# Kernel optimization log

Measured on AMD Instinct MI355X. Metric: run time of the kernel, lower is better.

## Reference

```python
import jax, jax.numpy as jnp
import numpy as np

DIM_V = 512
NUM_HEADS = 8
LN_EPS = 1e-5


def _layernorm(x):
    # LayerNorm over last dim, no affine (simplified_layer_norm=True)
    mu = jnp.mean(x, axis=-1, keepdims=True)
    var = jnp.mean(jnp.square(x - mu), axis=-1, keepdims=True)
    return (x - mu) * jax.lax.rsqrt(var + LN_EPS)


def setup_inputs() -> dict:
    key = jax.random.key(0)
    ks = jax.random.split(key, 12)
    B, Nq, Nk, dQ, dK, dV = 16, 1024, 1024, 512, 512, DIM_V
    s = 0.02
    return {
        "Q": jax.random.normal(ks[0], (B, Nq, dQ), jnp.float32),
        "K": jax.random.normal(ks[1], (B, Nk, dK), jnp.float32),
        "Wq": jax.random.normal(ks[2], (dQ, dV), jnp.float32) * s,
        "bq": jnp.zeros((dV,), jnp.float32),
        "Wk": jax.random.normal(ks[3], (dK, dV), jnp.float32) * s,
        "bk": jnp.zeros((dV,), jnp.float32),
        "Wv": jax.random.normal(ks[4], (dK, dV), jnp.float32) * s,
        "bv": jnp.zeros((dV,), jnp.float32),
        "Wo": jax.random.normal(ks[5], (dV, dV), jnp.float32) * s,
        "bo": jnp.zeros((dV,), jnp.float32),
    }


def reference(Q, K, Wq, bq, Wk, bk, Wv, bv, Wo, bo):
    H = NUM_HEADS
    dh = DIM_V // H
    q = Q @ Wq + bq            # [B, Nq, dV]
    k = K @ Wk + bk            # [B, Nk, dV]
    v = K @ Wv + bv            # [B, Nk, dV]
    B, Nq, _ = q.shape
    Nk = k.shape[1]
    qh = q.reshape(B, Nq, H, dh)
    kh = k.reshape(B, Nk, H, dh)
    vh = v.reshape(B, Nk, H, dh)
    # NOTE: faithful to source — scale by sqrt(dim_V), not sqrt(head_dim)
    scores = jnp.einsum('bqhd,bkhd->bhqk', qh, kh) / jnp.sqrt(jnp.asarray(DIM_V, q.dtype))
    A = jax.nn.softmax(scores, axis=-1)                    # [B, H, Nq, Nk]
    attn = jnp.einsum('bhqk,bkhd->bqhd', A, vh).reshape(B, Nq, DIM_V)
    O = q + attn               # residual with projected Q
    O = _layernorm(O)          # ln0 (no affine)
    O = O + jax.nn.gelu(O @ Wo + bo, approximate=False)
    O = _layernorm(O)          # ln1 (no affine)
    return O
```

## Files before the change

### kernel.cpp

```cpp
#include <hip/hip_runtime.h>
#include <hip/hip_bf16.h>
#include <math.h>

typedef __bf16 bf16;
typedef __bf16 bf16x8 __attribute__((ext_vector_type(8)));
typedef __bf16 bf16x4 __attribute__((ext_vector_type(4)));
typedef float  f32x4  __attribute__((ext_vector_type(4)));

#define MFMA16(a,b,c) __builtin_amdgcn_mfma_f32_16x16x32_bf16((a),(b),(c),0,0,0)
#define ATT_SCALE 0.0441941738241592f

__device__ __forceinline__ void async16(const bf16* g, bf16* l) {
    __builtin_amdgcn_global_load_lds((const __attribute__((address_space(1))) void*)g,
                                     (__attribute__((address_space(3))) void*)l,
                                     16, 0, 0);
}

__global__ __launch_bounds__(256) void prep_kernel(
    const float* __restrict__ Q, const float* __restrict__ K,
    const float* __restrict__ Wq, const float* __restrict__ Wk,
    const float* __restrict__ Wv, const float* __restrict__ Wo,
    bf16* __restrict__ Qb, bf16* __restrict__ Kb,
    bf16* __restrict__ WqT, bf16* __restrict__ WkT,
    bf16* __restrict__ WvT, bf16* __restrict__ WoT)
{
    __shared__ float tile[32][33];
    const int bx = blockIdx.x;
    if (bx < 8192) {
        const float* src = (bx < 4096) ? Q : K;
        bf16* dst        = (bx < 4096) ? Qb : Kb;
        int i = ((bx & 4095) * 256 + threadIdx.x) * 8;
        float4 a = *(const float4*)(src + i);
        float4 b = *(const float4*)(src + i + 4);
        bf16x8 o;
        o[0]=(bf16)a.x; o[1]=(bf16)a.y; o[2]=(bf16)a.z; o[3]=(bf16)a.w;
        o[4]=(bf16)b.x; o[5]=(bf16)b.y; o[6]=(bf16)b.z; o[7]=(bf16)b.w;
        *(bf16x8*)(dst + i) = o;
    } else {
        const int wid = bx - 8192;
        const float* W; bf16* T;
        switch (wid >> 8) {
          case 0: W=Wq; T=WqT; break;
          case 1: W=Wk; T=WkT; break;
          case 2: W=Wv; T=WvT; break;
          default: W=Wo; T=WoT; break;
        }
        const int rest = wid & 255;
        const int k0 = (rest & 15) * 32, n0 = (rest >> 4) * 32;
        const int tx = threadIdx.x & 31, ty = threadIdx.x >> 5;
        #pragma unroll
        for (int i=0;i<32;i+=8)
            tile[ty+i][tx] = W[(size_t)(k0+ty+i)*512 + n0+tx];
        __syncthreads();
        #pragma unroll
        for (int i=0;i<32;i+=8)
            T[(size_t)(n0+ty+i)*512 + k0+tx] = (bf16)tile[tx][ty+i];
    }
}

__device__ __forceinline__ void gemm_bt_body(
    const bf16* __restrict__ A, const bf16* __restrict__ BT,
    const float* __restrict__ bias,
    float* __restrict__ Cf, bf16* __restrict__ Cb, bf16* __restrict__ CvT)
{
    __shared__ bf16 As[128][32];
    __shared__ bf16 Bs[128][32];
    __shared__ bf16 Lt[64][136];
    const int m0 = blockIdx.x * 128, n0 = blockIdx.y * 128;
    const int tid = threadIdx.x;
    const int lane = tid & 63, wave = tid >> 6;
    const int qd = lane >> 4, lr = lane & 15;
    const int wm = (wave & 1) * 64, wn = (wave >> 1) * 64;

    const bf16* gA = A  + (size_t)(m0 + (tid>>2))*512 + (tid&3)*8;
    const bf16* gB = BT + (size_t)(n0 + (tid>>2))*512 + (tid&3)*8;
    bf16* lA = &As[0][0] + wave*512;
    bf16* lB = &Bs[0][0] + wave*512;

    f32x4 acc[4][4];
    #pragma unroll
    for (int i=0;i<4;i++)
      #pragma unroll
      for (int j=0;j<4;j++) acc[i][j] = (f32x4){0.f,0.f,0.f,0.f};

    for (int k0 = 0; k0 < 512; k0 += 32) {
        __syncthreads();
        async16(gA + k0,            lA);
        async16(gA + 64*512 + k0,   lA + 2048);
        async16(gB + k0,            lB);
        async16(gB + 64*512 + k0,   lB + 2048);
        __syncthreads();
        bf16x8 af[4], bfr[4];
        #pragma unroll
        for (int mi=0;mi<4;mi++) af[mi]  = *(bf16x8*)(&As[wm + mi*16 + lr][qd*8]);
        #pragma unroll
        for (int ni=0;ni<4;ni++) bfr[ni] = *(bf16x8*)(&Bs[wn + ni*16 + lr][qd*8]);
        #pragma unroll
        for (int mi=0;mi<4;mi++)
          #pragma unroll
          for (int ni=0;ni<4;ni++)
            acc[mi][ni] = MFMA16(af[mi], bfr[ni], acc[mi][ni]);
    }

    if (Cf || Cb) {
        #pragma unroll
        for (int ni=0;ni<4;ni++) {
            int n = n0 + wn + ni*16 + lr;
            float bv = bias[n];
            #pragma unroll
            for (int mi=0;mi<4;mi++) {
                int mb = m0 + wm + mi*16 + qd*4;
                #pragma unroll
                for (int r=0;r<4;r++) {
                    float v = acc[mi][ni][r] + bv;
                    if (Cf) Cf[(size_t)(mb+r)*512 + n] = v;
                    if (Cb) Cb[(size_t)(mb+r)*512 + n] = (bf16)v;
                }
            }
        }
    }
    if (CvT) {
        const int b = m0 >> 10, tok0 = m0 & 1023;
        const int row = tid >> 2, ch = tid & 3;
        #pragma unroll
        for (int half = 0; half < 2; ++half) {
            __syncthreads();
            if ((wn >> 6) == half) {
                #pragma unroll
                for (int ni=0;ni<4;ni++) {
                    int nl = ni*16 + lr;
                    float bv = bias[n0 + half*64 + nl];
                    #pragma unroll
                    for (int mi=0;mi<4;mi++)
                      #pragma unroll
                      for (int r=0;r<4;r++)
                        Lt[nl][wm + mi*16 + qd*4 + r] = (bf16)(acc[mi][ni][r] + bv);
                }
            }
            __syncthreads();
            const int h = (n0 >> 6) + half;
            uint4 x0 = *(uint4*)(&Lt[row][ch*32]);
            uint4 x1 = *(uint4*)(&Lt[row][ch*32 + 8]);
            bf16* dst = CvT + ((size_t)((b*8 + h)*64 + row))*1024 + tok0 + ch*32;
            *(uint4*)dst       = x0;
            *(uint4*)(dst + 8) = x1;
        }
    }
}

__global__ __launch_bounds__(256) void gemm_proj_kernel(
    const bf16* __restrict__ Qb, const bf16* __restrict__ Kb,
    const bf16* __restrict__ WqT, const bf16* __restrict__ WkT, const bf16* __restrict__ WvT,
    const float* __restrict__ bq, const float* __restrict__ bk, const float* __restrict__ bv,
    bf16* __restrict__ qbb, bf16* __restrict__ kbb, bf16* __restrict__ vT)
{
    switch (blockIdx.z) {
      case 0:  gemm_bt_body(Qb, WqT, bq, nullptr, qbb, nullptr); break;
      case 1:  gemm_bt_body(Kb, WkT, bk, nullptr, kbb, nullptr); break;
      default: gemm_bt_body(Kb, WvT, bv, nullptr, nullptr, vT); break;
    }
}

__global__ __launch_bounds__(256) void gemm_o_kernel(
    const bf16* __restrict__ Obf, const bf16* __restrict__ WoT,
    const float* __restrict__ bo, float* __restrict__ G32)
{
    gemm_bt_body(Obf, WoT, bo, G32, nullptr, nullptr);
}

__global__ __launch_bounds__(256, 4) void attn_kernel(
    const bf16* __restrict__ qb, const bf16* __restrict__ kb,
    const bf16* __restrict__ vT, bf16* __restrict__ attnb)
{
    const int qt = blockIdx.x, h = blockIdx.y, b = blockIdx.z;
    const int tid = threadIdx.x, lane = tid & 63, wave = tid >> 6;
    const int qd = lane >> 4, lr = lane & 15;
    const int q0 = qt*128 + wave*32;

    __shared__ bf16 Ks[64][72];
    __shared__ bf16 Vs[64][72];
    __shared__ bf16 Pl[4][32][72];

    bf16x8 aq[2][2];
    #pragma unroll
    for (int mi=0;mi<2;mi++) {
        const bf16* qrow = qb + ((size_t)(b*1024 + q0 + mi*16 + lr))*512 + h*64;
        aq[mi][0] = *(const bf16x8*)(qrow + qd*8);
        aq[mi][1] = *(const bf16x8*)(qrow + 32 + qd*8);
    }

    const int srow = tid >> 2;
    const int scol = (tid & 3) * 16;
    const bf16* kgp = kb + ((size_t)(b*1024 + srow))*512 + h*64 + scol;
    const bf16* vgp = vT + ((size_t)((b*8 + h)*64 + srow))*1024 + scol;

    uint4 k0r = *(const uint4*)(kgp);
    uint4 k1r = *(const uint4*)(kgp + 8);
    uint4 v0r = *(const uint4*)(vgp);
    uint4 v1r = *(const uint4*)(vgp + 8);

    f32x4 acc[2][4];
    #pragma unroll
    for (int mi=0;mi<2;mi++)
      #pragma unroll
      for (int ni=0;ni<4;ni++) acc[mi][ni] = (f32x4){0.f,0.f,0.f,0.f};
    float l[2][4] = {{0.f,0.f,0.f,0.f},{0.f,0.f,0.f,0.f}};

    for (int t=0; t<16; ++t) {
        __syncthreads();
        *(uint4*)(&Ks[srow][scol])   = k0r;
        *(uint4*)(&Ks[srow][scol+8]) = k1r;
        *(uint4*)(&Vs[srow][scol])   = v0r;
        *(uint4*)(&Vs[srow][scol+8]) = v1r;
        __syncthreads();
        if (t < 15) {
            const size_t ko = (size_t)(t+1)*64*512;
            const size_t vo = (size_t)(t+1)*64;
            k0r = *(const uint4*)(kgp + ko);
            k1r = *(const uint4*)(kgp + ko + 8);
            v0r = *(const uint4*)(vgp + vo);
            v1r = *(const uint4*)(vgp + vo + 8);
        }

        f32x4 s[2][4];
        #pragma unroll
        for (int mi=0;mi<2;mi++)
          #pragma unroll
          for (int ni=0;ni<4;ni++) s[mi][ni] = (f32x4){0.f,0.f,0.f,0.f};
        #pragma unroll
        for (int ni=0;ni<4;ni++) {
            bf16x8 b0 = *(bf16x8*)(&Ks[ni*16+lr][qd*8]);
            bf16x8 b1 = *(bf16x8*)(&Ks[ni*16+lr][32+qd*8]);
            #pragma unroll
            for (int mi=0;mi<2;mi++) {
                s[mi][ni] = MFMA16(aq[mi][0], b0, s[mi][ni]);
                s[mi][ni] = MFMA16(aq[mi][1], b1, s[mi][ni]);
            }
        }
        #pragma unroll
        for (int mi=0;mi<2;mi++)
          #pragma unroll
          for (int ni=0;ni<4;ni++)
            #pragma unroll
            for (int r=0;r<4;r++) {
                float pv = __expf(s[mi][ni][r] * ATT_SCALE);
                s[mi][ni][r] = pv;
                l[mi][r] += pv;
            }
        #pragma unroll
        for (int mi=0;mi<2;mi++)
          #pragma unroll
          for (int ni=0;ni<4;ni++)
            #pragma unroll
            for (int r=0;r<4;r++)
                Pl[wave][mi*16 + qd*4 + r][ni*16 + lr] = (bf16)s[mi][ni][r];
        bf16x8 ap[2][2];
        #pragma unroll
        for (int mi=0;mi<2;mi++) {
            ap[mi][0] = *(bf16x8*)(&Pl[wave][mi*16+lr][qd*8]);
            ap[mi][1] = *(bf16x8*)(&Pl[wave][mi*16+lr][32+qd*8]);
        }
        #pragma unroll
        for (int ni=0;ni<4;ni++) {
            bf16x8 v0 = *(bf16x8*)(&Vs[ni*16+lr][qd*8]);
            bf16x8 v1 = *(bf16x8*)(&Vs[ni*16+lr][32+qd*8]);
            #pragma unroll
            for (int mi=0;mi<2;mi++) {
                acc[mi][ni] = MFMA16(ap[mi][0], v0, acc[mi][ni]);
                acc[mi][ni] = MFMA16(ap[mi][1], v1, acc[mi][ni]);
            }
        }
    }

    #pragma unroll
    for (int off=1; off<16; off<<=1)
      #pragma unroll
      for (int mi=0;mi<2;mi++)
        #pragma unroll
        for (int r=0;r<4;r++) l[mi][r] += __shfl_xor(l[mi][r], off);

    #pragma unroll
    for (int mi=0;mi<2;mi++) {
        float inv[4];
        #pragma unroll
        for (int r=0;r<4;r++) inv[r] = 1.f / l[mi][r];
        #pragma unroll
        for (int ni=0;ni<4;ni++)
          #pragma unroll
          for (int r=0;r<4;r++)
            Pl[wave][qd*4+r][ni*16+lr] = (bf16)(acc[mi][ni][r] * inv[r]);
        bf16x8 oA = *(bf16x8*)(&Pl[wave][lr][qd*8]);
        bf16x8 oB = *(bf16x8*)(&Pl[wave][lr][32+qd*8]);
        bf16* dst = attnb + ((size_t)(b*1024 + q0 + mi*16 + lr))*512 + h*64;
        *(bf16x8*)(dst + qd*8)      = oA;
        *(bf16x8*)(dst + 32 + qd*8) = oB;
    }
}

__global__ __launch_bounds__(256) void ln0_kernel(
    const bf16* __restrict__ qbb, const bf16* __restrict__ attnb,
    bf16* __restrict__ Obf)
{
    const int wave = threadIdx.x >> 6, lane = threadIdx.x & 63;
    const int row = blockIdx.x*4 + wave;
    const size_t base = (size_t)row*512 + lane*8;
    bf16x8 qv = *(const bf16x8*)(qbb + base);
    bf16x8 av = *(const bf16x8*)(attnb + base);
    float x[8];
    #pragma unroll
    for (int i=0;i<8;i++) x[i] = (float)qv[i] + (float)av[i];
    float s1 = 0.f, s2 = 0.f;
    #pragma unroll
    for (int i=0;i<8;i++){ s1 += x[i]; s2 += x[i]*x[i]; }
    #pragma unroll
    for (int off=1; off<64; off<<=1) { s1 += __shfl_xor(s1, off); s2 += __shfl_xor(s2, off); }
    float mu  = s1 * (1.f/512.f);
    float var = s2 * (1.f/512.f) - mu*mu;
    float rstd = rsqrtf(var + 1e-5f);
    bf16x8 ob;
    #pragma unroll
    for (int i=0;i<8;i++) ob[i] = (bf16)((x[i]-mu)*rstd);
    *(bf16x8*)(Obf + base) = ob;
}

__global__ __launch_bounds__(256) void ln1_kernel(
    const bf16* __restrict__ Obf, const float* __restrict__ G32,
    float* __restrict__ out)
{
    const int wave = threadIdx.x >> 6, lane = threadIdx.x & 63;
    const int row = blockIdx.x*4 + wave;
    const size_t base = (size_t)row*512 + lane*8;
    bf16x8 ov = *(const bf16x8*)(Obf + base);
    float4 g0 = *(const float4*)(G32 + base);
    float4 g1 = *(const float4*)(G32 + base + 4);
    float gg[8] = {g0.x,g0.y,g0.z,g0.w,g1.x,g1.y,g1.z,g1.w};
    float x[8];
    #pragma unroll
    for (int i=0;i<8;i++) {
        float g = gg[i];
        float gelu = 0.5f * g * (1.f + erff(g * 0.70710678118654752f));
        x[i] = (float)ov[i] + gelu;
    }
    float s1 = 0.f, s2 = 0.f;
    #pragma unroll
    for (int i=0;i<8;i++){ s1 += x[i]; s2 += x[i]*x[i]; }
    #pragma unroll
    for (int off=1; off<64; off<<=1) { s1 += __shfl_xor(s1, off); s2 += __shfl_xor(s2, off); }
    float mu  = s1 * (1.f/512.f);
    float var = s2 * (1.f/512.f) - mu*mu;
    float rstd = rsqrtf(var + 1e-5f);
    float4 o0 = {(x[0]-mu)*rstd,(x[1]-mu)*rstd,(x[2]-mu)*rstd,(x[3]-mu)*rstd};
    float4 o1 = {(x[4]-mu)*rstd,(x[5]-mu)*rstd,(x[6]-mu)*rstd,(x[7]-mu)*rstd};
    *(float4*)(out + base)     = o0;
    *(float4*)(out + base + 4) = o1;
}

extern "C" void kernel_launch(void* const* d_in, const int* in_sizes, int n_in,
                              void* d_out, int out_size, void* d_ws, size_t ws_size,
                              hipStream_t stream)
{
    (void)in_sizes; (void)n_in; (void)out_size; (void)ws_size;
    const float* Q  = (const float*)d_in[0];
    const float* K  = (const float*)d_in[1];
    const float* Wq = (const float*)d_in[2];
    const float* bq = (const float*)d_in[3];
    const float* Wk = (const float*)d_in[4];
    const float* bk = (const float*)d_in[5];
    const float* Wv = (const float*)d_in[6];
    const float* bv = (const float*)d_in[7];
    const float* Wo = (const float*)d_in[8];
    const float* bo = (const float*)d_in[9];
    float* out = (float*)d_out;

    const size_t nTok = (size_t)16*1024*512;
    char* p = (char*)d_ws;
    auto alloc = [&](size_t bytes)->char* {
        char* r = p; p += (bytes + 255) & ~(size_t)255; return r;
    };
    bf16* Qb    = (bf16*)alloc(nTok*2);
    bf16* Kb    = (bf16*)alloc(nTok*2);
    bf16* WqT   = (bf16*)alloc(512*512*2);
    bf16* WkT   = (bf16*)alloc(512*512*2);
    bf16* WvT   = (bf16*)alloc(512*512*2);
    bf16* WoT   = (bf16*)alloc(512*512*2);
    bf16* qbb   = (bf16*)alloc(nTok*2);
    bf16* kbb   = (bf16*)alloc(nTok*2);
    bf16* vT    = (bf16*)alloc(nTok*2);
    bf16* attnb = (bf16*)alloc(nTok*2);
    bf16* Obf   = (bf16*)alloc(nTok*2);
    float* G32  = (float*)alloc(nTok*4);

    prep_kernel<<<9216, 256, 0, stream>>>(Q, K, Wq, Wk, Wv, Wo,
                                          Qb, Kb, WqT, WkT, WvT, WoT);
    gemm_proj_kernel<<<dim3(128,4,3), 256, 0, stream>>>(Qb, Kb, WqT, WkT, WvT,
                                                        bq, bk, bv, qbb, kbb, vT);
    attn_kernel<<<dim3(8,8,16), 256, 0, stream>>>(qbb, kbb, vT, attnb);
    ln0_kernel<<<4096, 256, 0, stream>>>(qbb, attnb, Obf);
    gemm_o_kernel<<<dim3(128,4), 256, 0, stream>>>(Obf, WoT, bo, G32);
    ln1_kernel<<<4096, 256, 0, stream>>>(Obf, G32, out);
}
```

Measured before the change: 277.2 us.

## Fuse input casts into QKV GEMM, share K tiles, swizzle LDS, fuse GELU

Drops the separate fp32-to-bf16 cast of Q and K. The QKV GEMM now loads fp32 A tiles directly into LDS through async global-to-LDS copies and converts them to bf16 on the fly. K and V projections share the same K input tile in one block with two accumulator sets. XOR swizzles are added to LDS layouts in all GEMMs and in attention, and attention moves to 16 query rows per wave with async K/V loads and twice as many blocks. GELU plus the residual add is fused into the output GEMM epilogue, which means an extra fp32 copy of the LN0 output is written and reread, and register pressure rises in the dual-accumulator GEMM.

New measurement: 286.4 us. 1.03x slower.

```diff
diff --git a/kernel.cpp b/kernel.cpp
--- a/kernel.cpp
+++ b/kernel.cpp
@@ -4,122 +4,133 @@
 
 typedef __bf16 bf16;
 typedef __bf16 bf16x8 __attribute__((ext_vector_type(8)));
-typedef __bf16 bf16x4 __attribute__((ext_vector_type(4)));
 typedef float  f32x4  __attribute__((ext_vector_type(4)));
 
 #define MFMA16(a,b,c) __builtin_amdgcn_mfma_f32_16x16x32_bf16((a),(b),(c),0,0,0)
 #define ATT_SCALE 0.0441941738241592f
 
-__device__ __forceinline__ void async16(const bf16* g, bf16* l) {
+__device__ __forceinline__ void async16p(const void* g, void* l) {
     __builtin_amdgcn_global_load_lds((const __attribute__((address_space(1))) void*)g,
                                      (__attribute__((address_space(3))) void*)l,
                                      16, 0, 0);
 }
 
-__global__ __launch_bounds__(256) void prep_kernel(
-    const float* __restrict__ Q, const float* __restrict__ K,
+__global__ __launch_bounds__(256) void prep_w_kernel(
     const float* __restrict__ Wq, const float* __restrict__ Wk,
     const float* __restrict__ Wv, const float* __restrict__ Wo,
-    bf16* __restrict__ Qb, bf16* __restrict__ Kb,
     bf16* __restrict__ WqT, bf16* __restrict__ WkT,
     bf16* __restrict__ WvT, bf16* __restrict__ WoT)
 {
     __shared__ float tile[32][33];
     const int bx = blockIdx.x;
-    if (bx < 8192) {
-        const float* src = (bx < 4096) ? Q : K;
-        bf16* dst        = (bx < 4096) ? Qb : Kb;
-        int i = ((bx & 4095) * 256 + threadIdx.x) * 8;
-        float4 a = *(const float4*)(src + i);
-        float4 b = *(const float4*)(src + i + 4);
-        bf16x8 o;
-        o[0]=(bf16)a.x; o[1]=(bf16)a.y; o[2]=(bf16)a.z; o[3]=(bf16)a.w;
-        o[4]=(bf16)b.x; o[5]=(bf16)b.y; o[6]=(bf16)b.z; o[7]=(bf16)b.w;
-        *(bf16x8*)(dst + i) = o;
-    } else {
-        const int wid = bx - 8192;
-        const float* W; bf16* T;
-        switch (wid >> 8) {
-          case 0: W=Wq; T=WqT; break;
-          case 1: W=Wk; T=WkT; break;
-          case 2: W=Wv; T=WvT; break;
-          default: W=Wo; T=WoT; break;
-        }
-        const int rest = wid & 255;
-        const int k0 = (rest & 15) * 32, n0 = (rest >> 4) * 32;
-        const int tx = threadIdx.x & 31, ty = threadIdx.x >> 5;
-        #pragma unroll
-        for (int i=0;i<32;i+=8)
-            tile[ty+i][tx] = W[(size_t)(k0+ty+i)*512 + n0+tx];
-        __syncthreads();
-        #pragma unroll
-        for (int i=0;i<32;i+=8)
-            T[(size_t)(n0+ty+i)*512 + k0+tx] = (bf16)tile[tx][ty+i];
-    }
-}
-
-__device__ __forceinline__ void gemm_bt_body(
-    const bf16* __restrict__ A, const bf16* __restrict__ BT,
-    const float* __restrict__ bias,
-    float* __restrict__ Cf, bf16* __restrict__ Cb, bf16* __restrict__ CvT)
-{
-    __shared__ bf16 As[128][32];
-    __shared__ bf16 Bs[128][32];
-    __shared__ bf16 Lt[64][136];
+    const float* W; bf16* T;
+    switch (bx >> 8) {
+      case 0: W=Wq; T=WqT; break;
+      case 1: W=Wk; T=WkT; break;
+      case 2: W=Wv; T=WvT; break;
+      default: W=Wo; T=WoT; break;
+    }
+    const int rest = bx & 255;
+    const int k0 = (rest & 15) * 32, n0 = (rest >> 4) * 32;
+    const int tx = threadIdx.x & 31, ty = threadIdx.x >> 5;
+    #pragma unroll
+    for (int i=0;i<32;i+=8)
+        tile[ty+i][tx] = W[(size_t)(k0+ty+i)*512 + n0+tx];
+    __syncthreads();
+    #pragma unroll
+    for (int i=0;i<32;i+=8)
+        T[(size_t)(n0+ty+i)*512 + k0+tx] = (bf16)tile[tx][ty+i];
+}
+
+__global__ __launch_bounds__(256, 2) void gemm_qkv_kernel(
+    const float* __restrict__ Qf, const float* __restrict__ Kf,
+    const bf16* __restrict__ WqT, const bf16* __restrict__ WkT,
+    const bf16* __restrict__ WvT,
+    const float* __restrict__ bq, const float* __restrict__ bk,
+    const float* __restrict__ bv,
+    bf16* __restrict__ qbb, bf16* __restrict__ kbb, bf16* __restrict__ vT)
+{
+    __shared__ float As32[128*32];
+    __shared__ bf16  Bs0[128*32];
+    __shared__ bf16  Bs1[128*32];
+    __shared__ bf16  Lt[64][136];
+    const bool kv = (blockIdx.z != 0);
+    const float* A   = kv ? Kf : Qf;
+    const bf16*  BT0 = kv ? WkT : WqT;
+    const float* b0  = kv ? bk : bq;
+    bf16* C0 = kv ? kbb : qbb;
+
     const int m0 = blockIdx.x * 128, n0 = blockIdx.y * 128;
     const int tid = threadIdx.x;
     const int lane = tid & 63, wave = tid >> 6;
     const int qd = lane >> 4, lr = lane & 15;
     const int wm = (wave & 1) * 64, wn = (wave >> 1) * 64;
 
-    const bf16* gA = A  + (size_t)(m0 + (tid>>2))*512 + (tid&3)*8;
-    const bf16* gB = BT + (size_t)(n0 + (tid>>2))*512 + (tid&3)*8;
-    bf16* lA = &As[0][0] + wave*512;
-    bf16* lB = &Bs[0][0] + wave*512;
-
-    f32x4 acc[4][4];
+    const float* gA = A + (size_t)(m0 + (tid>>3))*512 + (((tid&7)^((tid>>3)&7))*4);
+    float* lA = As32 + wave*256;
+    const int bgr = ((tid&3)^((tid>>2)&3))*8;
+    const bf16* gB0 = BT0 + (size_t)(n0 + (tid>>2))*512 + bgr;
+    const bf16* gB1 = WvT + (size_t)(n0 + (tid>>2))*512 + bgr;
+    bf16* lB0 = Bs0 + wave*512;
+    bf16* lB1 = Bs1 + wave*512;
+
+    f32x4 acc0[4][4], acc1[4][4];
     #pragma unroll
     for (int i=0;i<4;i++)
       #pragma unroll
-      for (int j=0;j<4;j++) acc[i][j] = (f32x4){0.f,0.f,0.f,0.f};
+      for (int j=0;j<4;j++) { acc0[i][j] = (f32x4){0,0,0,0}; acc1[i][j] = (f32x4){0,0,0,0}; }
 
     for (int k0 = 0; k0 < 512; k0 += 32) {
         __syncthreads();
-        async16(gA + k0,            lA);
-        async16(gA + 64*512 + k0,   lA + 2048);
-        async16(gB + k0,            lB);
-        async16(gB + 64*512 + k0,   lB + 2048);
-        __syncthreads();
-        bf16x8 af[4], bfr[4];
-        #pragma unroll
-        for (int mi=0;mi<4;mi++) af[mi]  = *(bf16x8*)(&As[wm + mi*16 + lr][qd*8]);
-        #pragma unroll
-        for (int ni=0;ni<4;ni++) bfr[ni] = *(bf16x8*)(&Bs[wn + ni*16 + lr][qd*8]);
+        #pragma unroll
+        for (int i=0;i<4;i++)
+            async16p(gA + k0 + (size_t)i*32*512, lA + i*1024);
+        async16p(gB0 + k0,            lB0);
+        async16p(gB0 + k0 + 64*512,   lB0 + 2048);
+        if (kv) {
+            async16p(gB1 + k0,          lB1);
+            async16p(gB1 + k0 + 64*512, lB1 + 2048);
+        }
+        __syncthreads();
+        bf16x8 af[4], bf0[4], bf1[4];
+        #pragma unroll
+        for (int mi=0;mi<4;mi++) {
+            int row = wm + mi*16 + lr;
+            f32x4 f0 = *(f32x4*)(As32 + row*32 + (((qd*2  )^(lr&7))*4));
+            f32x4 f1 = *(f32x4*)(As32 + row*32 + (((qd*2+1)^(lr&7))*4));
+            bf16x8 a;
+            a[0]=(bf16)f0[0]; a[1]=(bf16)f0[1]; a[2]=(bf16)f0[2]; a[3]=(bf16)f0[3];
+            a[4]=(bf16)f1[0]; a[5]=(bf16)f1[1]; a[6]=(bf16)f1[2]; a[7]=(bf16)f1[3];
+            af[mi] = a;
+        }
+        #pragma unroll
+        for (int ni=0;ni<4;ni++) {
+            int row = wn + ni*16 + lr;
+            bf0[ni] = *(bf16x8*)(Bs0 + row*32 + ((qd^(lr&3))*8));
+            if (kv) bf1[ni] = *(bf16x8*)(Bs1 + row*32 + ((qd^(lr&3))*8));
+        }
         #pragma unroll
         for (int mi=0;mi<4;mi++)
           #pragma unroll
-          for (int ni=0;ni<4;ni++)
-            acc[mi][ni] = MFMA16(af[mi], bfr[ni], acc[mi][ni]);
-    }
-
-    if (Cf || Cb) {
-        #pragma unroll
-        for (int ni=0;ni<4;ni++) {
-            int n = n0 + wn + ni*16 + lr;
-            float bv = bias[n];
+          for (int ni=0;ni<4;ni++) {
+            acc0[mi][ni] = MFMA16(af[mi], bf0[ni], acc0[mi][ni]);
+            if (kv) acc1[mi][ni] = MFMA16(af[mi], bf1[ni], acc1[mi][ni]);
+          }
+    }
+
+    #pragma unroll
+    for (int ni=0;ni<4;ni++) {
+        int n = n0 + wn + ni*16 + lr;
+        float bv0 = b0[n];
+        #pragma unroll
+        for (int mi=0;mi<4;mi++) {
+            int mb = m0 + wm + mi*16 + qd*4;
             #pragma unroll
-            for (int mi=0;mi<4;mi++) {
-                int mb = m0 + wm + mi*16 + qd*4;
-                #pragma unroll
-                for (int r=0;r<4;r++) {
-                    float v = acc[mi][ni][r] + bv;
-                    if (Cf) Cf[(size_t)(mb+r)*512 + n] = v;
-                    if (Cb) Cb[(size_t)(mb+r)*512 + n] = (bf16)v;
-                }
-            }
-        }
-    }
-    if (CvT) {
+            for (int r=0;r<4;r++)
+                C0[(size_t)(mb+r)*512 + n] = (bf16)(acc0[mi][ni][r] + bv0);
+        }
+    }
+    if (kv) {
         const int b = m0 >> 10, tok0 = m0 & 1023;
         const int row = tid >> 2, ch = tid & 3;
         #pragma unroll
@@ -129,43 +140,27 @@
                 #pragma unroll
                 for (int ni=0;ni<4;ni++) {
                     int nl = ni*16 + lr;
-                    float bv = bias[n0 + half*64 + nl];
+                    float bvv = bv[n0 + half*64 + nl];
                     #pragma unroll
                     for (int mi=0;mi<4;mi++)
                       #pragma unroll
                       for (int r=0;r<4;r++)
-                        Lt[nl][wm + mi*16 + qd*4 + r] = (bf16)(acc[mi][ni][r] + bv);
+                        Lt[nl][wm + mi*16 + qd*4 + r] = (bf16)(acc1[mi][ni][r] + bvv);
                 }
             }
             __syncthreads();
             const int h = (n0 >> 6) + half;
+            bf16* dst = vT + ((size_t)((b*8 + h)*64 + row))*1024 + tok0 + ch*32;
             uint4 x0 = *(uint4*)(&Lt[row][ch*32]);
             uint4 x1 = *(uint4*)(&Lt[row][ch*32 + 8]);
-            bf16* dst = CvT + ((size_t)((b*8 + h)*64 + row))*1024 + tok0 + ch*32;
-            *(uint4*)dst       = x0;
-            *(uint4*)(dst + 8) = x1;
-        }
-    }
-}
-
-__global__ __launch_bounds__(256) void gemm_proj_kernel(
-    const bf16* __restrict__ Qb, const bf16* __restrict__ Kb,
-    const bf16* __restrict__ WqT, const bf16* __restrict__ WkT, const bf16* __restrict__ WvT,
-    const float* __restrict__ bq, const float* __restrict__ bk, const float* __restrict__ bv,
-    bf16* __restrict__ qbb, bf16* __restrict__ kbb, bf16* __restrict__ vT)
-{
-    switch (blockIdx.z) {
-      case 0:  gemm_bt_body(Qb, WqT, bq, nullptr, qbb, nullptr); break;
-      case 1:  gemm_bt_body(Kb, WkT, bk, nullptr, kbb, nullptr); break;
-      default: gemm_bt_body(Kb, WvT, bv, nullptr, nullptr, vT); break;
-    }
-}
-
-__global__ __launch_bounds__(256) void gemm_o_kernel(
-    const bf16* __restrict__ Obf, const bf16* __restrict__ WoT,
-    const float* __restrict__ bo, float* __restrict__ G32)
-{
-    gemm_bt_body(Obf, WoT, bo, G32, nullptr, nullptr);
+            uint4 x2 = *(uint4*)(&Lt[row][ch*32 + 16]);
+            uint4 x3 = *(uint4*)(&Lt[row][ch*32 + 24]);
+            *(uint4*)(dst)      = x0;
+            *(uint4*)(dst + 8)  = x1;
+            *(uint4*)(dst + 16) = x2;
+            *(uint4*)(dst + 24) = x3;
+        }
+    }
 }
 
 __global__ __launch_bounds__(256, 4) void attn_kernel(
@@ -175,131 +170,99 @@
     const int qt = blockIdx.x, h = blockIdx.y, b = blockIdx.z;
     const int tid = threadIdx.x, lane = tid & 63, wave = tid >> 6;
     const int qd = lane >> 4, lr = lane & 15;
-    const int q0 = qt*128 + wave*32;
-
-    __shared__ bf16 Ks[64][72];
-    __shared__ bf16 Vs[64][72];
-    __shared__ bf16 Pl[4][32][72];
-
-    bf16x8 aq[2][2];
-    #pragma unroll
-    for (int mi=0;mi<2;mi++) {
-        const bf16* qrow = qb + ((size_t)(b*1024 + q0 + mi*16 + lr))*512 + h*64;
-        aq[mi][0] = *(const bf16x8*)(qrow + qd*8);
-        aq[mi][1] = *(const bf16x8*)(qrow + 32 + qd*8);
-    }
-
-    const int srow = tid >> 2;
-    const int scol = (tid & 3) * 16;
-    const bf16* kgp = kb + ((size_t)(b*1024 + srow))*512 + h*64 + scol;
-    const bf16* vgp = vT + ((size_t)((b*8 + h)*64 + srow))*1024 + scol;
-
-    uint4 k0r = *(const uint4*)(kgp);
-    uint4 k1r = *(const uint4*)(kgp + 8);
-    uint4 v0r = *(const uint4*)(vgp);
-    uint4 v1r = *(const uint4*)(vgp + 8);
-
-    f32x4 acc[2][4];
-    #pragma unroll
-    for (int mi=0;mi<2;mi++)
-      #pragma unroll
-      for (int ni=0;ni<4;ni++) acc[mi][ni] = (f32x4){0.f,0.f,0.f,0.f};
-    float l[2][4] = {{0.f,0.f,0.f,0.f},{0.f,0.f,0.f,0.f}};
+    const int q0 = qt*64 + wave*16;
+
+    __shared__ bf16 Ks[64*64];
+    __shared__ bf16 Vs[64*64];
+    __shared__ bf16 Pl[4][16][72];
+
+    bf16x8 aq0, aq1;
+    {
+        const bf16* qrow = qb + ((size_t)(b*1024 + q0 + lr))*512 + h*64;
+        aq0 = *(const bf16x8*)(qrow + qd*8);
+        aq1 = *(const bf16x8*)(qrow + 32 + qd*8);
+    }
+
+    const int srow = (tid >> 3) & 7;
+    const int sgr  = ((tid&7) ^ srow) * 8;
+    const bf16* kgp = kb + ((size_t)(b*1024 + wave*8 + srow))*512 + h*64 + sgr;
+    const bf16* vgp = vT + ((size_t)((b*8 + h)*64 + wave*8 + srow))*1024 + sgr;
+    bf16* lK = Ks + wave*512;
+    bf16* lV = Vs + wave*512;
+
+    f32x4 acc[4];
+    #pragma unroll
+    for (int i=0;i<4;i++) acc[i] = (f32x4){0,0,0,0};
+    float l[4] = {0.f,0.f,0.f,0.f};
 
     for (int t=0; t<16; ++t) {
-        __syncthreads();
-        *(uint4*)(&Ks[srow][scol])   = k0r;
-        *(uint4*)(&Ks[srow][scol+8]) = k1r;
-        *(uint4*)(&Vs[srow][scol])   = v0r;
-        *(uint4*)(&Vs[srow][scol+8]) = v1r;
-        __syncthreads();
-        if (t < 15) {
-            const size_t ko = (size_t)(t+1)*64*512;
-            const size_t vo = (size_t)(t+1)*64;
-            k0r = *(const uint4*)(kgp + ko);
-            k1r = *(const uint4*)(kgp + ko + 8);
-            v0r = *(const uint4*)(vgp + vo);
-            v1r = *(const uint4*)(vgp + vo + 8);
-        }
-
-        f32x4 s[2][4];
-        #pragma unroll
-        for (int mi=0;mi<2;mi++)
+        const int kk0 = t*64;
+        __syncthreads();
+        async16p(kgp + (size_t)kk0*512,            lK);
+        async16p(kgp + (size_t)(kk0+32)*512,       lK + 2048);
+        async16p(vgp + kk0,                        lV);
+        async16p(vgp + (size_t)32*1024 + kk0,      lV + 2048);
+        __syncthreads();
+
+        f32x4 s[4];
+        #pragma unroll
+        for (int ni=0;ni<4;ni++) s[ni] = (f32x4){0,0,0,0};
+        #pragma unroll
+        for (int ni=0;ni<4;ni++) {
+            int row = ni*16 + lr;
+            bf16x8 b0 = *(bf16x8*)(Ks + row*64 + (((qd  )^(lr&7))*8));
+            bf16x8 b1 = *(bf16x8*)(Ks + row*64 + (((qd+4)^(lr&7))*8));
+            s[ni] = MFMA16(aq0, b0, s[ni]);
+            s[ni] = MFMA16(aq1, b1, s[ni]);
+        }
+        #pragma unroll
+        for (int ni=0;ni<4;ni++)
           #pragma unroll
-          for (int ni=0;ni<4;ni++) s[mi][ni] = (f32x4){0.f,0.f,0.f,0.f};
-        #pragma unroll
-        for (int ni=0;ni<4;ni++) {
-            bf16x8 b0 = *(bf16x8*)(&Ks[ni*16+lr][qd*8]);
-            bf16x8 b1 = *(bf16x8*)(&Ks[ni*16+lr][32+qd*8]);
-            #pragma unroll
-            for (int mi=0;mi<2;mi++) {
-                s[mi][ni] = MFMA16(aq[mi][0], b0, s[mi][ni]);
-                s[mi][ni] = MFMA16(aq[mi][1], b1, s[mi][ni]);
-            }
-        }
-        #pragma unroll
-        for (int mi=0;mi<2;mi++)
-          #pragma unroll
-          for (int ni=0;ni<4;ni++)
-            #pragma unroll
-            for (int r=0;r<4;r++) {
-                float pv = __expf(s[mi][ni][r] * ATT_SCALE);
-                s[mi][ni][r] = pv;
-                l[mi][r] += pv;
-            }
-        #pragma unroll
-        for (int mi=0;mi<2;mi++)
-          #pragma unroll
-          for (int ni=0;ni<4;ni++)
-            #pragma unroll
-            for (int r=0;r<4;r++)
-                Pl[wave][mi*16 + qd*4 + r][ni*16 + lr] = (bf16)s[mi][ni][r];
-        bf16x8 ap[2][2];
-        #pragma unroll
-        for (int mi=0;mi<2;mi++) {
-            ap[mi][0] = *(bf16x8*)(&Pl[wave][mi*16+lr][qd*8]);
-            ap[mi][1] = *(bf16x8*)(&Pl[wave][mi*16+lr][32+qd*8]);
-        }
-        #pragma unroll
-        for (int ni=0;ni<4;ni++) {
-            bf16x8 v0 = *(bf16x8*)(&Vs[ni*16+lr][qd*8]);
-            bf16x8 v1 = *(bf16x8*)(&Vs[ni*16+lr][32+qd*8]);
-            #pragma unroll
-            for (int mi=0;mi<2;mi++) {
-                acc[mi][ni] = MFMA16(ap[mi][0], v0, acc[mi][ni]);
-                acc[mi][ni] = MFMA16(ap[mi][1], v1, acc[mi][ni]);
-            }
-        }
-    }
-
-    #pragma unroll
-    for (int off=1; off<16; off<<=1)
-      #pragma unroll
-      for (int mi=0;mi<2;mi++)
-        #pragma unroll
-        for (int r=0;r<4;r++) l[mi][r] += __shfl_xor(l[mi][r], off);
-
-    #pragma unroll
-    for (int mi=0;mi<2;mi++) {
-        float inv[4];
-        #pragma unroll
-        for (int r=0;r<4;r++) inv[r] = 1.f / l[mi][r];
+          for (int r=0;r<4;r++) {
+            float pv = __expf(s[ni][r] * ATT_SCALE);
+            s[ni][r] = pv;
+            l[r] += pv;
+          }
         #pragma unroll
         for (int ni=0;ni<4;ni++)
           #pragma unroll
           for (int r=0;r<4;r++)
-            Pl[wave][qd*4+r][ni*16+lr] = (bf16)(acc[mi][ni][r] * inv[r]);
-        bf16x8 oA = *(bf16x8*)(&Pl[wave][lr][qd*8]);
-        bf16x8 oB = *(bf16x8*)(&Pl[wave][lr][32+qd*8]);
-        bf16* dst = attnb + ((size_t)(b*1024 + q0 + mi*16 + lr))*512 + h*64;
-        *(bf16x8*)(dst + qd*8)      = oA;
-        *(bf16x8*)(dst + 32 + qd*8) = oB;
-    }
+            Pl[wave][qd*4+r][ni*16+lr] = (bf16)s[ni][r];
+        bf16x8 ap0 = *(bf16x8*)(&Pl[wave][lr][qd*8]);
+        bf16x8 ap1 = *(bf16x8*)(&Pl[wave][lr][32+qd*8]);
+        #pragma unroll
+        for (int ni=0;ni<4;ni++) {
+            int row = ni*16 + lr;
+            bf16x8 v0 = *(bf16x8*)(Vs + row*64 + (((qd  )^(lr&7))*8));
+            bf16x8 v1 = *(bf16x8*)(Vs + row*64 + (((qd+4)^(lr&7))*8));
+            acc[ni] = MFMA16(ap0, v0, acc[ni]);
+            acc[ni] = MFMA16(ap1, v1, acc[ni]);
+        }
+    }
+
+    #pragma unroll
+    for (int off=1; off<16; off<<=1)
+      #pragma unroll
+      for (int r=0;r<4;r++) l[r] += __shfl_xor(l[r], off);
+
+    float inv[4];
+    #pragma unroll
+    for (int r=0;r<4;r++) inv[r] = 1.f / l[r];
+    #pragma unroll
+    for (int ni=0;ni<4;ni++)
+      #pragma unroll
+      for (int r=0;r<4;r++)
+        Pl[wave][qd*4+r][ni*16+lr] = (bf16)(acc[ni][r] * inv[r]);
+    bf16x8 oA = *(bf16x8*)(&Pl[wave][lr][qd*8]);
+    bf16x8 oB = *(bf16x8*)(&Pl[wave][lr][32+qd*8]);
+    bf16* dst = attnb + ((size_t)(b*1024 + q0 + lr))*512 + h*64;
+    *(bf16x8*)(dst + qd*8)      = oA;
+    *(bf16x8*)(dst + 32 + qd*8) = oB;
 }
 
 __global__ __launch_bounds__(256) void ln0_kernel(
     const bf16* __restrict__ qbb, const bf16* __restrict__ attnb,
-    bf16* __restrict__ Obf)
+    bf16* __restrict__ Obf, float* __restrict__ O32)
 {
     const int wave = threadIdx.x >> 6, lane = threadIdx.x & 63;
     const int row = blockIdx.x*4 + wave;
@@ -317,30 +280,88 @@
     float mu  = s1 * (1.f/512.f);
     float var = s2 * (1.f/512.f) - mu*mu;
     float rstd = rsqrtf(var + 1e-5f);
-    bf16x8 ob;
-    #pragma unroll
-    for (int i=0;i<8;i++) ob[i] = (bf16)((x[i]-mu)*rstd);
+    bf16x8 ob; float4 o0, o1;
+    float y[8];
+    #pragma unroll
+    for (int i=0;i<8;i++) { y[i] = (x[i]-mu)*rstd; ob[i] = (bf16)y[i]; }
+    o0 = (float4){y[0],y[1],y[2],y[3]};
+    o1 = (float4){y[4],y[5],y[6],y[7]};
     *(bf16x8*)(Obf + base) = ob;
+    *(float4*)(O32 + base)     = o0;
+    *(float4*)(O32 + base + 4) = o1;
+}
+
+__global__ __launch_bounds__(256, 3) void gemm_o_kernel(
+    const bf16* __restrict__ Obf, const bf16* __restrict__ WoT,
+    const float* __restrict__ bo, const float* __restrict__ O32,
+    float* __restrict__ x32)
+{
+    __shared__ bf16 As[128*32];
+    __shared__ bf16 Bs[128*32];
+    const int m0 = blockIdx.x * 128, n0 = blockIdx.y * 128;
+    const int tid = threadIdx.x;
+    const int lane = tid & 63, wave = tid >> 6;
+    const int qd = lane >> 4, lr = lane & 15;
+    const int wm = (wave & 1) * 64, wn = (wave >> 1) * 64;
+
+    const int gr = ((tid&3)^((tid>>2)&3))*8;
+    const bf16* gA = Obf + (size_t)(m0 + (tid>>2))*512 + gr;
+    const bf16* gB = WoT + (size_t)(n0 + (tid>>2))*512 + gr;
+    bf16* lA = As + wave*512;
+    bf16* lB = Bs + wave*512;
+
+    f32x4 acc[4][4];
+    #pragma unroll
+    for (int i=0;i<4;i++)
+      #pragma unroll
+      for (int j=0;j<4;j++) acc[i][j] = (f32x4){0,0,0,0};
+
+    for (int k0 = 0; k0 < 512; k0 += 32) {
+        __syncthreads();
+        async16p(gA + k0,          lA);
+        async16p(gA + k0 + 64*512, lA + 2048);
+        async16p(gB + k0,          lB);
+        async16p(gB + k0 + 64*512, lB + 2048);
+        __syncthreads();
+        bf16x8 af[4], bfr[4];
+        #pragma unroll
+        for (int mi=0;mi<4;mi++) af[mi]  = *(bf16x8*)(As + (wm+mi*16+lr)*32 + ((qd^(lr&3))*8));
+        #pragma unroll
+        for (int ni=0;ni<4;ni++) bfr[ni] = *(bf16x8*)(Bs + (wn+ni*16+lr)*32 + ((qd^(lr&3))*8));
+        #pragma unroll
+        for (int mi=0;mi<4;mi++)
+          #pragma unroll
+          for (int ni=0;ni<4;ni++)
+            acc[mi][ni] = MFMA16(af[mi], bfr[ni], acc[mi][ni]);
+    }
+
+    #pragma unroll
+    for (int ni=0;ni<4;ni++) {
+        int n = n0 + wn + ni*16 + lr;
+        float bv = bo[n];
+        #pragma unroll
+        for (int mi=0;mi<4;mi++) {
+            int mb = m0 + wm + mi*16 + qd*4;
+            #pragma unroll
+            for (int r=0;r<4;r++) {
+                float g = acc[mi][ni][r] + bv;
+                float gelu = 0.5f * g * (1.f + erff(g * 0.70710678118654752f));
+                size_t idx = (size_t)(mb+r)*512 + n;
+                x32[idx] = O32[idx] + gelu;
+            }
+        }
+    }
 }
 
 __global__ __launch_bounds__(256) void ln1_kernel(
-    const bf16* __restrict__ Obf, const float* __restrict__ G32,
-    float* __restrict__ out)
+    const float* __restrict__ x32, float* __restrict__ out)
 {
     const int wave = threadIdx.x >> 6, lane = threadIdx.x & 63;
     const int row = blockIdx.x*4 + wave;
     const size_t base = (size_t)row*512 + lane*8;
-    bf16x8 ov = *(const bf16x8*)(Obf + base);
-    float4 g0 = *(const float4*)(G32 + base);
-    float4 g1 = *(const float4*)(G32 + base + 4);
-    float gg[8] = {g0.x,g0.y,g0.z,g0.w,g1.x,g1.y,g1.z,g1.w};
-    float x[8];
-    #pragma unroll
-    for (int i=0;i<8;i++) {
-        float g = gg[i];
-        float gelu = 0.5f * g * (1.f + erff(g * 0.70710678118654752f));
-        x[i] = (float)ov[i] + gelu;
-    }
+    float4 a0 = *(const float4*)(x32 + base);
+    float4 a1 = *(const float4*)(x32 + base + 4);
+    float x[8] = {a0.x,a0.y,a0.z,a0.w,a1.x,a1.y,a1.z,a1.w};
     float s1 = 0.f, s2 = 0.f;
     #pragma unroll
     for (int i=0;i<8;i++){ s1 += x[i]; s2 += x[i]*x[i]; }
@@ -377,8 +398,6 @@
     auto alloc = [&](size_t bytes)->char* {
         char* r = p; p += (bytes + 255) & ~(size_t)255; return r;
     };
-    bf16* Qb    = (bf16*)alloc(nTok*2);
-    bf16* Kb    = (bf16*)alloc(nTok*2);
     bf16* WqT   = (bf16*)alloc(512*512*2);
     bf16* WkT   = (bf16*)alloc(512*512*2);
     bf16* WvT   = (bf16*)alloc(512*512*2);
@@ -388,14 +407,14 @@
     bf16* vT    = (bf16*)alloc(nTok*2);
     bf16* attnb = (bf16*)alloc(nTok*2);
     bf16* Obf   = (bf16*)alloc(nTok*2);
-    float* G32  = (float*)alloc(nTok*4);
-
-    prep_kernel<<<9216, 256, 0, stream>>>(Q, K, Wq, Wk, Wv, Wo,
-                                          Qb, Kb, WqT, WkT, WvT, WoT);
-    gemm_proj_kernel<<<dim3(128,4,3), 256, 0, stream>>>(Qb, Kb, WqT, WkT, WvT,
-                                                        bq, bk, bv, qbb, kbb, vT);
-    attn_kernel<<<dim3(8,8,16), 256, 0, stream>>>(qbb, kbb, vT, attnb);
-    ln0_kernel<<<4096, 256, 0, stream>>>(qbb, attnb, Obf);
-    gemm_o_kernel<<<dim3(128,4), 256, 0, stream>>>(Obf, WoT, bo, G32);
-    ln1_kernel<<<4096, 256, 0, stream>>>(Obf, G32, out);
-}
+    float* O32  = (float*)alloc(nTok*4);
+    float* x32  = (float*)alloc(nTok*4);
+
+    prep_w_kernel<<<1024, 256, 0, stream>>>(Wq, Wk, Wv, Wo, WqT, WkT, WvT, WoT);
+    gemm_qkv_kernel<<<dim3(128,4,2), 256, 0, stream>>>(Q, K, WqT, WkT, WvT,
+                                                       bq, bk, bv, qbb, kbb, vT);
+    attn_kernel<<<dim3(16,8,16), 256, 0, stream>>>(qbb, kbb, vT, attnb);
+    ln0_kernel<<<4096, 256, 0, stream>>>(qbb, attnb, Obf, O32);
+    gemm_o_kernel<<<dim3(128,4), 256, 0, stream>>>(Obf, WoT, bo, O32, x32);
+    ln1_kernel<<<4096, 256, 0, stream>>>(x32, out);
+}
```
